# Kernel tuning notes

Hardware: AMD Instinct MI355X
Metric: run time of the kernel (lower is better)

The kernel has to match this reference:

```python
import jax, jax.numpy as jnp
import numpy as np

B, L, E, D, H, P, NL = 4, 2048, 7, 512, 8, 720, 2
DH = D // H
FACTOR = 5
U = min(L, FACTOR * int(np.ceil(np.log(L))))  # top-u queries, = 40
SCALE = 1.0 / np.sqrt(DH)


def setup_inputs() -> dict:
    key = jax.random.key(0)
    ks = jax.random.split(key, 12)
    s = 0.02
    rn = lambda k, shape: jax.random.normal(k, shape, jnp.float32) * s
    return {
        "x": jax.random.normal(ks[0], (B, L, E), jnp.float32),
        "emb_w": rn(ks[1], (E, D)), "emb_b": jnp.zeros((D,), jnp.float32),
        "Wq": rn(ks[2], (NL, D, D)), "bq": jnp.zeros((NL, D), jnp.float32),
        "Wk": rn(ks[3], (NL, D, D)), "bk": jnp.zeros((NL, D), jnp.float32),
        "Wv": rn(ks[4], (NL, D, D)), "bv": jnp.zeros((NL, D), jnp.float32),
        "Wo": rn(ks[5], (NL, D, D)), "bo": jnp.zeros((NL, D), jnp.float32),
        "W1": rn(ks[6], (NL, D, D)), "b1": jnp.zeros((NL, D), jnp.float32),
        "W2": rn(ks[7], (NL, D, D)), "b2": jnp.zeros((NL, D), jnp.float32),
        "ln1_g": jnp.ones((NL, D), jnp.float32), "ln1_b": jnp.zeros((NL, D), jnp.float32),
        "ln2_g": jnp.ones((NL, D), jnp.float32), "ln2_b": jnp.zeros((NL, D), jnp.float32),
        "proj_w": rn(ks[8], (D, E)), "proj_b": jnp.zeros((E,), jnp.float32),
    }


def layer_norm(x, g, b):
    m = jnp.mean(x, axis=-1, keepdims=True)
    v = jnp.mean(jnp.square(x - m), axis=-1, keepdims=True)
    return (x - m) * jax.lax.rsqrt(v + 1e-5) * g + b


def prob_sparse_attn(x, Wq, bq, Wk, bk, Wv, bv, Wo, bo):
    # x: [B, L, D] -> heads [B, H, L, DH]
    q = (x @ Wq + bq).reshape(B, L, H, DH).transpose(0, 2, 1, 3)
    k = (x @ Wk + bk).reshape(B, L, H, DH).transpose(0, 2, 1, 3)
    v = (x @ Wv + bv).reshape(B, L, H, DH).transpose(0, 2, 1, 3)
    scores = jnp.einsum('bhqd,bhkd->bhqk', q, k) * SCALE  # [B,H,L,L]
    # sparsity measure M(q) = max_k - mean_k
    M = jnp.max(scores, axis=-1) - jnp.mean(scores, axis=-1)  # [B,H,L]
    _, idx = jax.lax.top_k(M, U)  # [B,H,U] indices of active queries
    s_top = jnp.take_along_axis(scores, idx[..., None], axis=2)  # [B,H,U,L]
    attn = jax.nn.softmax(s_top, axis=-1)
    upd = jnp.einsum('bhul,bhld->bhud', attn, v)  # [B,H,U,DH]
    # lazy queries get the mean of V; active queries get attention output
    ctx = jnp.broadcast_to(jnp.mean(v, axis=2, keepdims=True), v.shape)
    bidx = jnp.arange(B)[:, None, None]
    hidx = jnp.arange(H)[None, :, None]
    ctx = ctx.at[bidx, hidx, idx].set(upd)  # scatter active queries
    out = ctx.transpose(0, 2, 1, 3).reshape(B, L, D)
    return out @ Wo + bo


def reference(x, emb_w, emb_b, Wq, bq, Wk, bk, Wv, bv, Wo, bo,
              W1, b1, W2, b2, ln1_g, ln1_b, ln2_g, ln2_b, proj_w, proj_b):
    h = x @ emb_w + emb_b  # [B,L,D]
    for i in range(NL):
        a = prob_sparse_attn(h, Wq[i], bq[i], Wk[i], bk[i], Wv[i], bv[i], Wo[i], bo[i])
        h = layer_norm(h + a, ln1_g[i], ln1_b[i])
        f = jax.nn.relu(h @ W1[i] + b1[i]) @ W2[i] + b2[i]
        h = layer_norm(h + f, ln2_g[i], ln2_b[i])
    return h[:, -P:, :] @ proj_w + proj_b  # [B,P,E]
```

## Files before the change

kernel.cpp:

```cpp
#include <hip/hip_runtime.h>
#include <hip/hip_bf16.h>
#include <cstdint>
#include <cstddef>

#define BB 4
#define LL 2048
#define EE 7
#define DD 512
#define HH 8
#define DHH 64
#define PP 720
#define NLAYER 2
#define UU 40
#define SCALE 0.125f
#define ROWS (BB*LL)
#define BIGN ((size_t)ROWS*DD)
#define NIN 21
#define FCH 256
#define NCH (LL/FCH)
#define PSTR 264
#define VSTR 136
#define WOFF 1280
#define WTPB 12
#define WRPB 768

typedef unsigned short u16;
typedef unsigned long long u64;
typedef __bf16 bf16x8 __attribute__((ext_vector_type(8)));
typedef float  f32x4  __attribute__((ext_vector_type(4)));

__device__ __forceinline__ float bf2f(u16 u){
  union { uint32_t i; float f; } c; c.i = ((uint32_t)u) << 16; return c.f;
}
__device__ __forceinline__ u16 f2b(float f){
  __hip_bfloat16 h = __float2bfloat16(f);
  return *(u16*)&h;
}
__device__ __forceinline__ void gld_lds16(const u16* g, u16* l){
  __builtin_amdgcn_global_load_lds(
      (const __attribute__((address_space(1))) uint32_t*)g,
      (__attribute__((address_space(3))) uint32_t*)l, 16, 0, 0);
}
__device__ __forceinline__ int is_bf16(const void* d15){
  return (*(const uint32_t*)d15 == 0x3F800000u) ? 0 : 1;
}

__device__ __forceinline__ void addln_row_vals(const u16* a, const u16* r,
    const float* g, const float* bvec, int row, int lane, u16 ob[8]){
  size_t base = (size_t)row * DD + lane*8;
  ushort4 a0 = *(const ushort4*)(a + base);
  ushort4 a1 = *(const ushort4*)(a + base + 4);
  ushort4 r0 = *(const ushort4*)(r + base);
  ushort4 r1 = *(const ushort4*)(r + base + 4);
  float x[8] = {bf2f(a0.x)+bf2f(r0.x), bf2f(a0.y)+bf2f(r0.y),
                bf2f(a0.z)+bf2f(r0.z), bf2f(a0.w)+bf2f(r0.w),
                bf2f(a1.x)+bf2f(r1.x), bf2f(a1.y)+bf2f(r1.y),
                bf2f(a1.z)+bf2f(r1.z), bf2f(a1.w)+bf2f(r1.w)};
  float s = 0.f;
  #pragma unroll
  for (int i=0;i<8;i++) s += x[i];
  #pragma unroll
  for (int off=1; off<64; off<<=1) s += __shfl_xor(s, off);
  float mean = s * (1.0f/DD);
  float vs = 0.f;
  #pragma unroll
  for (int i=0;i<8;i++){ x[i] -= mean; vs += x[i]*x[i]; }
  #pragma unroll
  for (int off=1; off<64; off<<=1) vs += __shfl_xor(vs, off);
  float rs = rsqrtf(vs * (1.0f/DD) + 1e-5f);
  const float* gp = g + lane*8;
  const float* bp = bvec + lane*8;
  #pragma unroll
  for (int i=0;i<8;i++) ob[i] = f2b(x[i]*rs*gp[i] + bp[i]);
}

__device__ __forceinline__ void tile_map(int flat, int tilesPerB, int winOff,
                                         int* mbRow, int* nbOut){
  int mq = tilesPerB >> 1;
  int xcd = flat & 7, rest = flat >> 3;
  int mbi = xcd + 8*(rest % mq);
  int bat = mbi / tilesPerB;
  *mbRow = bat*LL + winOff + (mbi - bat*tilesPerB)*64;
  *nbOut = (rest / mq) * 128;
}

#define NSMALL 15
struct ConvArgs { const void* src[NSMALL]; int off[NSMALL]; int n[NSMALL]; };
struct WPtrs { const void* p[6]; };

__global__ __launch_bounds__(256) void k_preamble(ConvArgs a, WPtrs wp,
    const void* __restrict__ xraw, const void* __restrict__ d15,
    float* __restrict__ dst, float* __restrict__ zbuf,
    u16* __restrict__ hB, u16* __restrict__ wT){
  int y = blockIdx.y, bx = blockIdx.x, t = threadIdx.x;
  int isbf = is_bf16(d15);
  __shared__ u16 tile[64][65];
  __shared__ float xs[32][EE];
  if (y < NSMALL){
    int i = bx*256 + t;
    if (i >= a.n[y]) return;
    float v;
    if (isbf) v = bf2f(((const u16*)a.src[y])[i]);
    else      v = ((const float*)a.src[y])[i];
    dst[(size_t)a.off[y] + i] = v;
  } else if (y == NSMALL){
    int i = bx*256 + t;
    if (i < NLAYER*4096) zbuf[i] = 0.f;
  } else if (y < 32){
    int flat = (y - 16)*256 + bx;
    if (flat >= 512) return;
    int colgrp = flat & 1;
    int rowbase = (flat >> 1) * 32;
    int dd = colgrp*256 + t;
    if (t < 32*EE){
      int j = t / EE, e = t - j*EE;
      xs[j][e] = isbf ? bf2f(((const u16*)xraw)[(rowbase + j)*EE + e])
                      : ((const float*)xraw)[(rowbase + j)*EE + e];
    }
    float wreg[EE];
    #pragma unroll
    for (int e=0;e<EE;e++)
      wreg[e] = isbf ? bf2f(((const u16*)a.src[1])[e*DD + dd])
                     : ((const float*)a.src[1])[e*DD + dd];
    float bias = isbf ? bf2f(((const u16*)a.src[2])[dd]) : ((const float*)a.src[2])[dd];
    __syncthreads();
    for (int j=0;j<32;j++){
      float acc = bias;
      #pragma unroll
      for (int e=0;e<EE;e++) acc = fmaf(xs[j][e], wreg[e], acc);
      hB[(size_t)(rowbase + j)*DD + dd] = f2b(acc);
    }
  } else {
    int flat = (y - 32)*256 + bx;
    int mz = flat >> 6, tl = flat & 63;
    int lay = mz / 6, mat = mz % 6;
    int n0 = (tl & 7)*64, k0 = (tl >> 3)*64;
    int r = t >> 6, c = t & 63;
    const void* src = wp.p[mat];
    for (int rr = r; rr < 64; rr += 4){
      size_t idx = ((size_t)lay*DD + (k0+rr))*DD + n0 + c;
      u16 v;
      if (isbf) v = ((const u16*)src)[idx];
      else      v = f2b(((const float*)src)[idx]);
      tile[rr][c] = v;
    }
    __syncthreads();
    u16* drow = wT + ((size_t)mz*DD + n0)*DD + k0;
    int c4 = (t & 15)*4;
    for (int rr = (t >> 4); rr < 64; rr += 16){
      ushort4 v = { tile[c4][rr], tile[c4+1][rr], tile[c4+2][rr], tile[c4+3][rr] };
      *(ushort4*)(drow + (size_t)rr*DD + c4) = v;
    }
  }
}

__global__ __launch_bounds__(256) void k_gemm_mfma(const u16* __restrict__ A, const u16* __restrict__ Bt,
    const float* __restrict__ bias, u16* __restrict__ Cb, int relu,
    int tilesPerB, int winOff){
  __shared__ u16 As[64*64];
  __shared__ u16 Bs[128*64];
  int t = threadIdx.x, wave = t >> 6, lane = t & 63;
  int qlane = lane & 15, quad = lane >> 4;
  int flat = blockIdx.x + gridDim.x*blockIdx.y;
  int mb, nb;
  tile_map(flat, tilesPerB, winOff, &mb, &nb);
  int wm = (wave & 1) * 32, wn = (wave >> 1) * 64;
  f32x4 acc[2][4];
  #pragma unroll
  for (int i=0;i<2;i++)
    #pragma unroll
    for (int j=0;j<4;j++) acc[i][j] = (f32x4){0.f,0.f,0.f,0.f};

  int srow = wave*8 + (lane>>3);
  int scol = (((lane&7) ^ ((lane>>3)&7))) * 8;
  const u16* Ag = A + (size_t)(mb + srow)*DD + scol;
  const u16* Bg = Bt + (size_t)(nb + srow)*DD + scol;

  for (int k0 = 0; k0 < DD; k0 += 64){
    __syncthreads();
    #pragma unroll
    for (int i=0;i<2;i++)
      gld_lds16(Ag + (size_t)i*32*DD + k0, As + (i*32 + wave*8)*64);
    #pragma unroll
    for (int i=0;i<4;i++)
      gld_lds16(Bg + (size_t)i*32*DD + k0, Bs + (i*32 + wave*8)*64);
    __syncthreads();
    #pragma unroll
    for (int ch=0; ch<2; ++ch){
      bf16x8 af[2], bfv[4];
      int cgL = ((ch*4 + quad) ^ (qlane & 7)) * 8;
      #pragma unroll
      for (int i=0;i<2;i++) af[i] = *(const bf16x8*)(As + (wm + i*16 + qlane)*64 + cgL);
      #pragma unroll
      for (int j=0;j<4;j++) bfv[j] = *(const bf16x8*)(Bs + (wn + j*16 + qlane)*64 + cgL);
      #pragma unroll
      for (int i=0;i<2;i++)
        #pragma unroll
        for (int j=0;j<4;j++)
          acc[i][j] = __builtin_amdgcn_mfma_f32_16x16x32_bf16(af[i], bfv[j], acc[i][j], 0, 0, 0);
    }
  }
  #pragma unroll
  for (int i=0;i<2;i++){
    int rbase = mb + wm + i*16 + quad*4;
    #pragma unroll
    for (int j=0;j<4;j++){
      int col = nb + wn + j*16 + qlane;
      float bv = bias[col];
      #pragma unroll
      for (int r=0;r<4;r++){
        float cv = acc[i][j][r] + bv;
        if (relu) cv = fmaxf(cv, 0.f);
        Cb[(size_t)(rbase + r)*DD + col] = f2b(cv);
      }
    }
  }
}

__global__ __launch_bounds__(256) void k_gemm_wo(const u64* __restrict__ rowPtr, const u16* __restrict__ Bt,
    const float* __restrict__ bias, u16* __restrict__ Cb,
    int tilesPerB, int winOff){
  __shared__ u16 As[64*64];
  __shared__ u16 Bs[128*64];
  int t = threadIdx.x, wave = t >> 6, lane = t & 63;
  int qlane = lane & 15, quad = lane >> 4;
  int flat = blockIdx.x + gridDim.x*blockIdx.y;
  int mb, nb;
  tile_map(flat, tilesPerB, winOff, &mb, &nb);
  int wm = (wave & 1) * 32, wn = (wave >> 1) * 64;
  f32x4 acc[2][4];
  #pragma unroll
  for (int i=0;i<2;i++)
    #pragma unroll
    for (int j=0;j<4;j++) acc[i][j] = (f32x4){0.f,0.f,0.f,0.f};

  int srow = wave*8 + (lane>>3);
  int scol = (((lane&7) ^ ((lane>>3)&7))) * 8;
  const u16* Bg = Bt + (size_t)(nb + srow)*DD + scol;

  for (int k0 = 0; k0 < DD; k0 += 64){
    int slice = k0 >> 6;
    __syncthreads();
    #pragma unroll
    for (int i=0;i<2;i++){
      int arow = mb + i*32 + srow;
      const u16* src = (const u16*)(uintptr_t)rowPtr[(size_t)arow*8 + slice] + scol;
      gld_lds16(src, As + (i*32 + wave*8)*64);
    }
    #pragma unroll
    for (int i=0;i<4;i++)
      gld_lds16(Bg + (size_t)i*32*DD + k0, Bs + (i*32 + wave*8)*64);
    __syncthreads();
    #pragma unroll
    for (int ch=0; ch<2; ++ch){
      bf16x8 af[2], bfv[4];
      int cgL = ((ch*4 + quad) ^ (qlane & 7)) * 8;
      #pragma unroll
      for (int i=0;i<2;i++) af[i] = *(const bf16x8*)(As + (wm + i*16 + qlane)*64 + cgL);
      #pragma unroll
      for (int j=0;j<4;j++) bfv[j] = *(const bf16x8*)(Bs + (wn + j*16 + qlane)*64 + cgL);
      #pragma unroll
      for (int i=0;i<2;i++)
        #pragma unroll
        for (int j=0;j<4;j++)
          acc[i][j] = __builtin_amdgcn_mfma_f32_16x16x32_bf16(af[i], bfv[j], acc[i][j], 0, 0, 0);
    }
  }
  #pragma unroll
  for (int i=0;i<2;i++){
    int rbase = mb + wm + i*16 + quad*4;
    #pragma unroll
    for (int j=0;j<4;j++){
      int col = nb + wn + j*16 + qlane;
      float bv = bias[col];
      #pragma unroll
      for (int r=0;r<4;r++){
        float cv = acc[i][j][r] + bv;
        Cb[(size_t)(rbase + r)*DD + col] = f2b(cv);
      }
    }
  }
}

__global__ __launch_bounds__(256) void k_gemm_qkv(const u16* __restrict__ A, const u16* __restrict__ Wt,
    const float* __restrict__ bq, const float* __restrict__ bk, const float* __restrict__ bv,
    u16* __restrict__ qB, u16* __restrict__ kB, u16* __restrict__ vB,
    float* __restrict__ ksum, float* __restrict__ vsum){
  __shared__ u16 As[128*64];
  __shared__ u16 Bs[128*64];
  int t = threadIdx.x, wave = t >> 6, lane = t & 63;
  int qlane = lane & 15, quad = lane >> 4;
  int flat = blockIdx.x + gridDim.x*blockIdx.y;
  int xcd = flat & 7, rest = flat >> 3;
  int mb  = (xcd + 8*(rest & 7)) * 128;
  int nbg = (rest >> 3) * 128;
  int sel = nbg >> 9;
  int nb  = nbg & 511;
  const float* bias = (sel==0) ? bq : (sel==1) ? bk : bv;
  u16* out = (sel==0) ? qB : (sel==1) ? kB : vB;
  const u16* Bt = Wt + (size_t)sel*DD*DD;
  int wm = (wave & 1) * 64, wn = (wave >> 1) * 64;
  f32x4 acc[4][4];
  #pragma unroll
  for (int i=0;i<4;i++)
    #pragma unroll
    for (int j=0;j<4;j++) acc[i][j] = (f32x4){0.f,0.f,0.f,0.f};

  int srow = wave*8 + (lane>>3);
  int scol = (((lane&7) ^ ((lane>>3)&7))) * 8;
  const u16* Ag = A + (size_t)(mb + srow)*DD + scol;
  const u16* Bg = Bt + (size_t)(nb + srow)*DD + scol;

  for (int k0 = 0; k0 < DD; k0 += 64){
    __syncthreads();
    #pragma unroll
    for (int i=0;i<4;i++){
      gld_lds16(Ag + (size_t)i*32*DD + k0, As + (i*32 + wave*8)*64);
      gld_lds16(Bg + (size_t)i*32*DD + k0, Bs + (i*32 + wave*8)*64);
    }
    __syncthreads();
    #pragma unroll
    for (int ch=0; ch<2; ++ch){
      bf16x8 af[4], bf[4];
      int cgL = ((ch*4 + quad) ^ (qlane & 7)) * 8;
      #pragma unroll
      for (int i=0;i<4;i++) af[i] = *(const bf16x8*)(As + (wm + i*16 + qlane)*64 + cgL);
      #pragma unroll
      for (int j=0;j<4;j++) bf[j] = *(const bf16x8*)(Bs + (wn + j*16 + qlane)*64 + cgL);
      #pragma unroll
      for (int i=0;i<4;i++)
        #pragma unroll
        for (int j=0;j<4;j++)
          acc[i][j] = __builtin_amdgcn_mfma_f32_16x16x32_bf16(af[i], bf[j], acc[i][j], 0, 0, 0);
    }
  }
  float csum[4] = {0.f,0.f,0.f,0.f};
  #pragma unroll
  for (int j=0;j<4;j++){
    int col = nb + wn + j*16 + qlane;
    float bvv = bias[col];
    #pragma unroll
    for (int i=0;i<4;i++){
      int rbase = mb + wm + i*16 + quad*4;
      #pragma unroll
      for (int r=0;r<4;r++){
        float cv = acc[i][j][r] + bvv;
        out[(size_t)(rbase + r)*DD + col] = f2b(cv);
        csum[j] += cv;
      }
    }
  }
  if (sel > 0){
    float* dst = (sel==1) ? ksum : vsum;
    int bidx = mb >> 11;
    #pragma unroll
    for (int j=0;j<4;j++){
      float v = csum[j];
      v += __shfl_xor(v, 16);
      v += __shfl_xor(v, 32);
      if ((lane>>4) == 0)
        atomicAdd(dst + bidx*512 + nb + wn + j*16 + lane, v);
    }
  }
}

__global__ __launch_bounds__(256) void k_sparsity_mfma(const u16* __restrict__ qB, const u16* __restrict__ kB,
    const float* __restrict__ ksum, float* __restrict__ Mout){
  int flat = blockIdx.x + gridDim.x*blockIdx.y;
  int xcd = flat & 7, rest = flat >> 3;
  int qc = rest & 15;
  int bh = (rest >> 4)*8 + xcd;
  int b = bh >> 3, hh = bh & 7;
  int q0 = qc * 128;
  int t = threadIdx.x, wave = t >> 6, lane = t & 63;
  const u16* qbase = qB + ((size_t)(b*LL + q0))*DD + hh*DHH;
  const u16* kbase = kB + ((size_t)b*LL)*DD + hh*DHH;
  bf16x8 qa[8][2];
  #pragma unroll
  for (int i=0;i<8;i++)
    #pragma unroll
    for (int c=0;c<2;c++)
      qa[i][c] = *(const bf16x8*)(qbase + (size_t)(i*16 + (lane&15))*DD + c*32 + (lane>>4)*8);
  float rmax[8][4];
  #pragma unroll
  for (int i=0;i<8;i++)
    #pragma unroll
    for (int r=0;r<4;r++) rmax[i][r] = -3.0e38f;
  for (int kt = wave*16; kt < LL; kt += 64){
    bf16x8 kb0 = *(const bf16x8*)(kbase + (size_t)(kt + (lane&15))*DD + (lane>>4)*8);
    bf16x8 kb1 = *(const bf16x8*)(kbase + (size_t)(kt + (lane&15))*DD + 32 + (lane>>4)*8);
    #pragma unroll
    for (int i=0;i<8;i++){
      f32x4 a = (f32x4){0.f,0.f,0.f,0.f};
      a = __builtin_amdgcn_mfma_f32_16x16x32_bf16(qa[i][0], kb0, a, 0, 0, 0);
      a = __builtin_amdgcn_mfma_f32_16x16x32_bf16(qa[i][1], kb1, a, 0, 0, 0);
      #pragma unroll
      for (int r=0;r<4;r++) rmax[i][r] = fmaxf(rmax[i][r], a[r]);
    }
  }
  #pragma unroll
  for (int i=0;i<8;i++)
    #pragma unroll
    for (int r=0;r<4;r++){
      float v = rmax[i][r];
      v = fmaxf(v, __shfl_xor(v, 1));
      v = fmaxf(v, __shfl_xor(v, 2));
      v = fmaxf(v, __shfl_xor(v, 4));
      v = fmaxf(v, __shfl_xor(v, 8));
      rmax[i][r] = v;
    }
  __shared__ float smax[4][128];
  if ((lane & 15) == 0){
    #pragma unroll
    for (int i=0;i<8;i++)
      #pragma unroll
      for (int r=0;r<4;r++)
        smax[wave][i*16 + (lane>>4)*4 + r] = rmax[i][r];
  }
  __syncthreads();
  if (t < 128){
    float mx = fmaxf(fmaxf(smax[0][t], smax[1][t]), fmaxf(smax[2][t], smax[3][t]));
    const u16* qrow = qB + (size_t)(b*LL + q0 + t)*DD + hh*DHH;
    float dot = 0.f;
    #pragma unroll
    for (int dv=0; dv<16; ++dv){
      ushort4 qv = *(const ushort4*)(qrow + dv*4);
      const float* kp = ksum + bh*DHH + dv*4;
      dot += bf2f(qv.x)*kp[0] + bf2f(qv.y)*kp[1]
           + bf2f(qv.z)*kp[2] + bf2f(qv.w)*kp[3];
    }
    Mout[bh*LL + q0 + t] = SCALE * (mx - dot * (1.0f/LL));
  }
}

__global__ __launch_bounds__(256) void k_flash(const u16* __restrict__ qB, const u16* __restrict__ kB,
    const u16* __restrict__ vB, const float* __restrict__ Mv, int* __restrict__ sidx,
    float* __restrict__ pO, float* __restrict__ pM, float* __restrict__ pS){
  int bh = blockIdx.y, c = blockIdx.x;
  int b = bh >> 3, hh = bh & 7;
  int t = threadIdx.x, w = t >> 6, lane = t & 63;
  int qlane = lane & 15, quad = lane >> 4;
  int l0 = c * FCH;
  __shared__ u16 Ps[48*PSTR];
  __shared__ union { uint32_t keys[LL]; u16 vst[64*VSTR]; } uu;
  __shared__ float wred[4][48];
  __shared__ float mrow[48];
  __shared__ int hist[256];
  __shared__ int scr[2];
  __shared__ int tieIdx[64];
  __shared__ int counters[2];
  __shared__ int sidxL[UU], sidxS[UU];

  {
    const float* src = Mv + (size_t)bh*LL;
    #pragma unroll
    for (int j = 0; j < 8; ++j){
      int idx = t + j*256;
      uint32_t u = __float_as_uint(src[idx]);
      uu.keys[idx] = (u & 0x80000000u) ? ~u : (u | 0x80000000u);
    }
    uint32_t prefix = 0, pmask = 0;
    int need = UU;
    #pragma unroll
    for (int pass = 0; pass < 4; ++pass){
      int shift = 24 - pass*8;
      __syncthreads();
      hist[t] = 0;
      __syncthreads();
      #pragma unroll
      for (int j = 0; j < 8; ++j){
        uint32_t k = uu.keys[t + j*256];
        if ((k & pmask) == prefix)
          atomicAdd(&hist[(k >> shift) & 0xFF], 1);
      }
      __syncthreads();
      if (t < 64){
        int ln = t;
        int h0 = hist[ln*4+0], h1 = hist[ln*4+1], h2 = hist[ln*4+2], h3 = hist[ln*4+3];
        int s = h0 + h1 + h2 + h3;
        int acc = s;
        #pragma unroll
        for (int off = 1; off < 64; off <<= 1){
          int v = __shfl_down(acc, off);
          if (ln + off < 64) acc += v;
        }
        int c3 = acc - s;
        int c2 = c3 + h3;
        int c1 = c2 + h2;
        int c0 = c1 + h1;
        if      (need > c3 && need <= c3 + h3){ scr[0] = ln*4+3; scr[1] = c3; }
        else if (need > c2 && need <= c2 + h2){ scr[0] = ln*4+2; scr[1] = c2; }
        else if (need > c1 && need <= c1 + h1){ scr[0] = ln*4+1; scr[1] = c1; }
        else if (need > c0 && need <= c0 + h0){ scr[0] = ln*4+0; scr[1] = c0; }
      }
      __syncthreads();
      prefix |= ((uint32_t)scr[0]) << shift;
      need -= scr[1];
      pmask |= 0xFFu << shift;
    }
    if (t < 2) counters[t] = 0;
    __syncthreads();
    uint32_t Tkey = prefix;
    #pragma unroll
    for (int j = 0; j < 8; ++j){
      int idx = t + j*256;
      uint32_t k = uu.keys[idx];
      if (k > Tkey){
        int p = atomicAdd(&counters[0], 1);
        sidxL[p] = idx;
      } else if (k == Tkey){
        int p = atomicAdd(&counters[1], 1);
        if (p < 64) tieIdx[p] = idx;
      }
    }
    __syncthreads();
    if (t == 0){
      int c_gt = counters[0];
      int tc = counters[1];
      int needTies = UU - c_gt;
      if (tc <= 64){
        for (int m = 0; m < needTies; ++m){
          int bestv = 0x7FFFFFFF, bestp = -1;
          for (int q = 0; q < tc; ++q)
            if (tieIdx[q] < bestv){ bestv = tieIdx[q]; bestp = q; }
          sidxL[c_gt + m] = bestv;
          tieIdx[bestp] = 0x7FFFFFFF;
        }
      } else {
        int m = 0;
        for (int j = 0; j < LL && m < needTies; ++j)
          if (uu.keys[j] == Tkey){ sidxL[c_gt + m] = j; m++; }
      }
    }
    __syncthreads();
    int vv = 0, rk = 0;
    if (t < UU){
      vv = sidxL[t];
      #pragma unroll 8
      for (int j = 0; j < UU; ++j) rk += (sidxL[j] < vv) ? 1 : 0;
    }
    __syncthreads();
    if (t < UU) sidxS[rk] = vv;
    __syncthreads();
    if (c == 0 && t < UU) sidx[bh*UU + t] = sidxS[t];
  }

  const u16* kbase = kB + (size_t)b*LL*DD + hh*DHH;
  const u16* vbase = vB + (size_t)b*LL*DD + hh*DHH;
  const u16* qbase = qB + (size_t)b*LL*DD + hh*DHH;

  bf16x8 qa[3][2];
  #pragma unroll
  for (int i=0;i<3;i++){
    int u = i*16 + qlane;
    if (u < UU){
      const u16* qr = qbase + (size_t)sidxS[u]*DD + quad*8;
      qa[i][0] = *(const bf16x8*)qr;
      qa[i][1] = *(const bf16x8*)(qr + 32);
    } else {
      bf16x8 z;
      #pragma unroll
      for (int q8=0;q8<8;q8++) z[q8] = (__bf16)0.0f;
      qa[i][0] = z; qa[i][1] = z;
    }
  }
  f32x4 S[3][4];
  #pragma unroll
  for (int j=0;j<4;j++){
    const u16* kr = kbase + (size_t)(l0 + w*64 + j*16 + qlane)*DD + quad*8;
    bf16x8 k0 = *(const bf16x8*)kr;
    bf16x8 k1 = *(const bf16x8*)(kr + 32);
    #pragma unroll
    for (int i=0;i<3;i++){
      f32x4 a = (f32x4){0.f,0.f,0.f,0.f};
      a = __builtin_amdgcn_mfma_f32_16x16x32_bf16(qa[i][0], k0, a, 0, 0, 0);
      a = __builtin_amdgcn_mfma_f32_16x16x32_bf16(qa[i][1], k1, a, 0, 0, 0);
      S[i][j] = a;
    }
  }
  #pragma unroll
  for (int i=0;i<3;i++){
    #pragma unroll
    for (int r=0;r<4;r++){
      float m = -3.0e38f;
      #pragma unroll
      for (int j=0;j<4;j++){ S[i][j][r] *= SCALE; m = fmaxf(m, S[i][j][r]); }
      m = fmaxf(m, __shfl_xor(m, 1));
      m = fmaxf(m, __shfl_xor(m, 2));
      m = fmaxf(m, __shfl_xor(m, 4));
      m = fmaxf(m, __shfl_xor(m, 8));
      if (qlane == 0) wred[w][i*16 + quad*4 + r] = m;
    }
  }
  __syncthreads();
  if (t < 48) mrow[t] = fmaxf(fmaxf(wred[0][t], wred[1][t]), fmaxf(wred[2][t], wred[3][t]));
  __syncthreads();
  #pragma unroll
  for (int i=0;i<3;i++){
    #pragma unroll
    for (int r=0;r<4;r++){
      int row = i*16 + quad*4 + r;
      float m = mrow[row];
      float ls = 0.f;
      #pragma unroll
      for (int j=0;j<4;j++){
        float e = __expf(S[i][j][r] - m);
        ls += e;
        Ps[row*PSTR + w*64 + j*16 + qlane] = f2b(e);
      }
      ls += __shfl_xor(ls, 1);
      ls += __shfl_xor(ls, 2);
      ls += __shfl_xor(ls, 4);
      ls += __shfl_xor(ls, 8);
      if (qlane == 0) wred[w][row] = ls;
    }
  }
  __syncthreads();
  if (t < 48){
    pM[(bh*NCH + c)*48 + t] = mrow[t];
    pS[(bh*NCH + c)*48 + t] = wred[0][t] + wred[1][t] + wred[2][t] + wred[3][t];
  }
  f32x4 O[3];
  #pragma unroll
  for (int i=0;i<3;i++) O[i] = (f32x4){0.f,0.f,0.f,0.f};
  for (int half = 0; half < 2; ++half){
    __syncthreads();
    for (int idx = t; idx < 128*64; idx += 256){
      int rr = idx >> 6, d = idx & 63;
      uu.vst[d*VSTR + rr] = vbase[(size_t)(l0 + half*128 + rr)*DD + d];
    }
    __syncthreads();
    #pragma unroll
    for (int ks = 0; ks < 4; ++ks){
      int kloc = half*128 + ks*32;
      bf16x8 bfv = *(const bf16x8*)(uu.vst + (w*16 + qlane)*VSTR + ks*32 + quad*8);
      #pragma unroll
      for (int i=0;i<3;i++){
        bf16x8 af = *(const bf16x8*)(Ps + (i*16 + qlane)*PSTR + kloc + quad*8);
        O[i] = __builtin_amdgcn_mfma_f32_16x16x32_bf16(af, bfv, O[i], 0, 0, 0);
      }
    }
  }
  size_t ob = (size_t)(bh*NCH + c)*48*64;
  #pragma unroll
  for (int i=0;i<3;i++)
    #pragma unroll
    for (int r=0;r<4;r++)
      pO[ob + (size_t)(i*16 + quad*4 + r)*64 + w*16 + qlane] = O[i][r];
}

__global__ __launch_bounds__(256) void k_flash_red(const float* __restrict__ pO, const float* __restrict__ pM,
    const float* __restrict__ pS, const int* __restrict__ sidx, const float* __restrict__ vsum,
    u16* __restrict__ attnC, u16* __restrict__ vmeanB, u64* __restrict__ rowPtr){
  int bh = blockIdx.x; int b = bh >> 3, hh = bh & 7;
  int t = threadIdx.x;
  if (t < 64) vmeanB[b*512 + hh*64 + t] = f2b(vsum[b*512 + hh*64 + t] * (1.0f/LL));
  u64 vmPtr = (u64)(uintptr_t)(vmeanB + b*512 + hh*64);
  for (int row = t; row < LL; row += 256)
    rowPtr[((size_t)b*LL + row)*8 + hh] = vmPtr;
  __syncthreads();
  if (t < UU)
    rowPtr[((size_t)b*LL + sidx[bh*UU + t])*8 + hh] =
        (u64)(uintptr_t)(attnC + ((size_t)bh*UU + t)*64);
  for (int idx = t; idx < UU*64; idx += 256){
    int u = idx >> 6, n = idx & 63;
    float m = -3.0e38f;
    #pragma unroll
    for (int c=0;c<NCH;c++) m = fmaxf(m, pM[(bh*NCH + c)*48 + u]);
    float s = 0.f, o = 0.f;
    #pragma unroll
    for (int c=0;c<NCH;c++){
      float wgt = __expf(pM[(bh*NCH + c)*48 + u] - m);
      s += wgt * pS[(bh*NCH + c)*48 + u];
      o += wgt * pO[((size_t)(bh*NCH + c)*48 + u)*64 + n];
    }
    attnC[((size_t)bh*UU + u)*64 + n] = f2b(o / s);
  }
}

__global__ __launch_bounds__(256) void k_addln(const u16* __restrict__ a, const u16* __restrict__ r,
    const float* __restrict__ g, const float* __restrict__ bvec, u16* __restrict__ outB,
    int rowsPerB, int winOff){
  int g0 = blockIdx.x*4 + (threadIdx.x >> 6);
  int lane = threadIdx.x & 63;
  int bat = g0 / rowsPerB;
  int row = bat*LL + winOff + (g0 - bat*rowsPerB);
  u16 ob[8];
  addln_row_vals(a, r, g, bvec, row, lane, ob);
  size_t base = (size_t)row * DD + lane*8;
  *(ushort4*)(outB + base)     = (ushort4){ob[0],ob[1],ob[2],ob[3]};
  *(ushort4*)(outB + base + 4) = (ushort4){ob[4],ob[5],ob[6],ob[7]};
}

__global__ __launch_bounds__(256) void k_proj_ln(const u16* __restrict__ hIn, const u16* __restrict__ res,
    const float* __restrict__ lng, const float* __restrict__ lnbv,
    const float* __restrict__ pw, const float* __restrict__ pb,
    void* __restrict__ out, const void* __restrict__ d15){
  int w = threadIdx.x >> 6, lane = threadIdx.x & 63;
  int rp = blockIdx.x*4 + w;
  int b = rp / PP, pp = rp - b*PP;
  int row = b*LL + (LL-PP) + pp;
  u16 ob[8];
  addln_row_vals(hIn, res, lng, lnbv, row, lane, ob);
  float x[8];
  #pragma unroll
  for (int j=0;j<8;j++) x[j] = bf2f(ob[j]);
  float acc[EE];
  #pragma unroll
  for (int e=0;e<EE;e++) acc[e]=0.f;
  #pragma unroll
  for (int j=0;j<8;j++){
    const float* wrow = pw + (size_t)(lane*8 + j)*EE;
    #pragma unroll
    for (int e=0;e<EE;e++) acc[e] = fmaf(x[j], wrow[e], acc[e]);
  }
  int isbf = is_bf16(d15);
  #pragma unroll
  for (int e=0;e<EE;e++){
    float rr = acc[e];
    #pragma unroll
    for (int off=32; off>0; off>>=1) rr += __shfl_down(rr, off);
    if (lane == 0){
      float val = rr + pb[e];
      if (isbf) ((__hip_bfloat16*)out)[(size_t)rp*EE + e] = __float2bfloat16(val);
      else      ((float*)out)[(size_t)rp*EE + e] = val;
    }
  }
}

extern "C" void kernel_launch(void* const* d_in, const int* in_sizes, int n_in,
                              void* d_out, int out_size, void* d_ws, size_t ws_size,
                              hipStream_t stream){
  float* ws    = (float*)d_ws;
  float* Mv    = ws;
  float* ksumL = Mv + (size_t)BB*HH*LL;
  float* pM    = ksumL + NLAYER*4096;
  float* pS    = pM + 12288;
  float* pO    = pS + 12288;
  int*   sidx  = (int*)(pO + 786432);
  u64*   rowPtr= (u64*)(((uintptr_t)(sidx + 1280) + 15) & ~(uintptr_t)15);
  u16*   attnC = (u16*)(rowPtr + (size_t)ROWS*8);
  u16*   vmeanB= attnC + (size_t)BB*HH*UU*64;
  u16*   hB    = vmeanB + 2048;
  u16*   qB    = hB + BIGN;
  u16*   kB    = qB + BIGN;
  u16*   vB    = kB + BIGN;
  u16*   f1B   = vB + BIGN;
  u16*   tmpB  = f1B + BIGN;
  u16*   wT    = tmpB + BIGN;
  float* conv  = (float*)(((uintptr_t)(wT + (size_t)12*DD*DD) + 15) & ~(uintptr_t)15);

  static const int small_ids[NSMALL] = {0,1,2,4,6,8,10,12,14,15,16,17,18,19,20};
  ConvArgs ca;
  int off_all[NIN];
  int tot = 0;
  for (int i = 0; i < NIN; ++i) off_all[i] = -1;
  for (int s = 0; s < NSMALL; ++s){
    int i = small_ids[s];
    ca.src[s] = d_in[i];
    ca.off[s] = tot;
    ca.n[s]   = in_sizes[i];
    off_all[i] = tot;
    tot += in_sizes[i];
  }
  const float* bq = conv + off_all[4];
  const float* bk = conv + off_all[6];
  const float* bv = conv + off_all[8];
  const float* bo = conv + off_all[10];
  const float* b1 = conv + off_all[12];
  const float* b2 = conv + off_all[14];
  const float* ln1g = conv + off_all[15]; const float* ln1b = conv + off_all[16];
  const float* ln2g = conv + off_all[17]; const float* ln2b = conv + off_all[18];
  const float* pw = conv + off_all[19]; const float* pb = conv + off_all[20];

  WPtrs wp;
  wp.p[0]=d_in[3]; wp.p[1]=d_in[5]; wp.p[2]=d_in[7];
  wp.p[3]=d_in[9]; wp.p[4]=d_in[11]; wp.p[5]=d_in[13];

  k_preamble<<<dim3(256, 35), 256, 0, stream>>>(ca, wp, d_in[0], d_in[15],
                                                conv, ksumL, hB, wT);

  dim3 gg0(4, 128);
  dim3 gg1(4, WTPB*BB);
  dim3 gq(3*DD/128, ROWS/128);

  for (int l = 0; l < NLAYER; ++l){
    const u16* WqkvT = wT + (size_t)(l*6 + 0)*DD*DD;
    const u16* WoT   = wT + (size_t)(l*6 + 3)*DD*DD;
    const u16* W1T   = wT + (size_t)(l*6 + 4)*DD*DD;
    const u16* W2T   = wT + (size_t)(l*6 + 5)*DD*DD;
    float* ksum = ksumL + l*4096;
    float* vsum = ksum + 2048;

    k_gemm_qkv<<<gq, 256, 0, stream>>>(hB, WqkvT, bq + l*DD, bk + l*DD, bv + l*DD,
                                       qB, kB, vB, ksum, vsum);
    k_sparsity_mfma<<<dim3(LL/128, BB*HH), 256, 0, stream>>>(qB, kB, ksum, Mv);
    k_flash<<<dim3(NCH, BB*HH), 256, 0, stream>>>(qB, kB, vB, Mv, sidx, pO, pM, pS);
    k_flash_red<<<BB*HH, 256, 0, stream>>>(pO, pM, pS, sidx, vsum, attnC, vmeanB, rowPtr);
    if (l < NLAYER - 1){
      k_gemm_wo<<<gg0, 256, 0, stream>>>(rowPtr, WoT, bo + l*DD, tmpB, 32, 0);
      k_addln<<<ROWS/4, 256, 0, stream>>>(hB, tmpB, ln1g + l*DD, ln1b + l*DD, hB, LL, 0);
      k_gemm_mfma<<<gg0, 256, 0, stream>>>(hB, W1T, b1 + l*DD, f1B, 1, 32, 0);
      k_gemm_mfma<<<gg0, 256, 0, stream>>>(f1B, W2T, b2 + l*DD, tmpB, 0, 32, 0);
      k_addln<<<ROWS/4, 256, 0, stream>>>(hB, tmpB, ln2g + l*DD, ln2b + l*DD, hB, LL, 0);
    } else {
      k_gemm_wo<<<gg1, 256, 0, stream>>>(rowPtr, WoT, bo + l*DD, tmpB, WTPB, WOFF);
      k_addln<<<(WRPB*BB)/4, 256, 0, stream>>>(hB, tmpB, ln1g + l*DD, ln1b + l*DD, hB,
                                               WRPB, WOFF);
      k_gemm_mfma<<<gg1, 256, 0, stream>>>(hB, W1T, b1 + l*DD, f1B, 1, WTPB, WOFF);
      k_gemm_mfma<<<gg1, 256, 0, stream>>>(f1B, W2T, b2 + l*DD, tmpB, 0, WTPB, WOFF);
      k_proj_ln<<<(BB*PP)/4, 256, 0, stream>>>(hB, tmpB, ln2g + l*DD, ln2b + l*DD,
                                               pw, pb, d_out, d_in[15]);
    }
  }
}
```

Baseline: 348.2 us.

## Fuse Q/K/V tiles per block in QKV GEMM and vectorize V staging

The QKV GEMM used 128x128 tiles, each covering one of Q, K or V. Now each block computes a 128-row by 64-column tile for all three at once, so the A tile is loaded once and reused across the Q, K and V weights. The grid goes from 12x64 to 8x64 blocks, each with more work, and the kernel holds 24 accumulators in place of 16, which may raise register pressure. Separately, the V transpose staging in the flash kernel now reads 8 elements per thread with vector loads instead of scalar loads.

```diff
diff --git a/kernel.cpp b/kernel.cpp
--- a/kernel.cpp
+++ b/kernel.cpp
@@ -287,79 +287,88 @@
     u16* __restrict__ qB, u16* __restrict__ kB, u16* __restrict__ vB,
     float* __restrict__ ksum, float* __restrict__ vsum){
   __shared__ u16 As[128*64];
-  __shared__ u16 Bs[128*64];
+  __shared__ u16 Bs[3][64*64];
   int t = threadIdx.x, wave = t >> 6, lane = t & 63;
   int qlane = lane & 15, quad = lane >> 4;
   int flat = blockIdx.x + gridDim.x*blockIdx.y;
   int xcd = flat & 7, rest = flat >> 3;
   int mb  = (xcd + 8*(rest & 7)) * 128;
-  int nbg = (rest >> 3) * 128;
-  int sel = nbg >> 9;
-  int nb  = nbg & 511;
-  const float* bias = (sel==0) ? bq : (sel==1) ? bk : bv;
-  u16* out = (sel==0) ? qB : (sel==1) ? kB : vB;
-  const u16* Bt = Wt + (size_t)sel*DD*DD;
-  int wm = (wave & 1) * 64, wn = (wave >> 1) * 64;
-  f32x4 acc[4][4];
-  #pragma unroll
-  for (int i=0;i<4;i++)
-    #pragma unroll
-    for (int j=0;j<4;j++) acc[i][j] = (f32x4){0.f,0.f,0.f,0.f};
+  int nb  = (rest >> 3) * 64;
+  int wm  = wave * 32;
+  f32x4 acc[3][2][4];
+  #pragma unroll
+  for (int s=0;s<3;s++)
+    #pragma unroll
+    for (int i=0;i<2;i++)
+      #pragma unroll
+      for (int j=0;j<4;j++) acc[s][i][j] = (f32x4){0.f,0.f,0.f,0.f};
 
   int srow = wave*8 + (lane>>3);
   int scol = (((lane&7) ^ ((lane>>3)&7))) * 8;
   const u16* Ag = A + (size_t)(mb + srow)*DD + scol;
-  const u16* Bg = Bt + (size_t)(nb + srow)*DD + scol;
+  const u16* Bg = Wt + (size_t)(nb + srow)*DD + scol;
 
   for (int k0 = 0; k0 < DD; k0 += 64){
     __syncthreads();
     #pragma unroll
-    for (int i=0;i<4;i++){
+    for (int i=0;i<4;i++)
       gld_lds16(Ag + (size_t)i*32*DD + k0, As + (i*32 + wave*8)*64);
-      gld_lds16(Bg + (size_t)i*32*DD + k0, Bs + (i*32 + wave*8)*64);
-    }
+    #pragma unroll
+    for (int s=0;s<3;s++)
+      #pragma unroll
+      for (int i=0;i<2;i++)
+        gld_lds16(Bg + (size_t)s*DD*DD + (size_t)i*32*DD + k0, Bs[s] + (i*32 + wave*8)*64);
     __syncthreads();
     #pragma unroll
     for (int ch=0; ch<2; ++ch){
-      bf16x8 af[4], bf[4];
       int cgL = ((ch*4 + quad) ^ (qlane & 7)) * 8;
-      #pragma unroll
-      for (int i=0;i<4;i++) af[i] = *(const bf16x8*)(As + (wm + i*16 + qlane)*64 + cgL);
-      #pragma unroll
-      for (int j=0;j<4;j++) bf[j] = *(const bf16x8*)(Bs + (wn + j*16 + qlane)*64 + cgL);
-      #pragma unroll
-      for (int i=0;i<4;i++)
+      bf16x8 af[2];
+      #pragma unroll
+      for (int i=0;i<2;i++) af[i] = *(const bf16x8*)(As + (wm + i*16 + qlane)*64 + cgL);
+      #pragma unroll
+      for (int s=0;s<3;s++){
+        bf16x8 bf[4];
         #pragma unroll
-        for (int j=0;j<4;j++)
-          acc[i][j] = __builtin_amdgcn_mfma_f32_16x16x32_bf16(af[i], bf[j], acc[i][j], 0, 0, 0);
-    }
-  }
-  float csum[4] = {0.f,0.f,0.f,0.f};
-  #pragma unroll
-  for (int j=0;j<4;j++){
-    int col = nb + wn + j*16 + qlane;
-    float bvv = bias[col];
-    #pragma unroll
-    for (int i=0;i<4;i++){
-      int rbase = mb + wm + i*16 + quad*4;
-      #pragma unroll
-      for (int r=0;r<4;r++){
-        float cv = acc[i][j][r] + bvv;
-        out[(size_t)(rbase + r)*DD + col] = f2b(cv);
-        csum[j] += cv;
-      }
-    }
-  }
-  if (sel > 0){
-    float* dst = (sel==1) ? ksum : vsum;
-    int bidx = mb >> 11;
+        for (int j=0;j<4;j++) bf[j] = *(const bf16x8*)(Bs[s] + (j*16 + qlane)*64 + cgL);
+        #pragma unroll
+        for (int i=0;i<2;i++)
+          #pragma unroll
+          for (int j=0;j<4;j++)
+            acc[s][i][j] = __builtin_amdgcn_mfma_f32_16x16x32_bf16(af[i], bf[j], acc[s][i][j], 0, 0, 0);
+      }
+    }
+  }
+  #pragma unroll
+  for (int s=0;s<3;s++){
+    const float* bias = (s==0) ? bq : (s==1) ? bk : bv;
+    u16* out = (s==0) ? qB : (s==1) ? kB : vB;
+    float csum[4] = {0.f,0.f,0.f,0.f};
     #pragma unroll
     for (int j=0;j<4;j++){
-      float v = csum[j];
-      v += __shfl_xor(v, 16);
-      v += __shfl_xor(v, 32);
-      if ((lane>>4) == 0)
-        atomicAdd(dst + bidx*512 + nb + wn + j*16 + lane, v);
+      int col = nb + j*16 + qlane;
+      float bvv = bias[col];
+      #pragma unroll
+      for (int i=0;i<2;i++){
+        int rbase = mb + wm + i*16 + quad*4;
+        #pragma unroll
+        for (int r=0;r<4;r++){
+          float cv = acc[s][i][j][r] + bvv;
+          out[(size_t)(rbase + r)*DD + col] = f2b(cv);
+          csum[j] += cv;
+        }
+      }
+    }
+    if (s > 0){
+      float* dst = (s==1) ? ksum : vsum;
+      int bidx = mb >> 11;
+      #pragma unroll
+      for (int j=0;j<4;j++){
+        float v = csum[j];
+        v += __shfl_xor(v, 16);
+        v += __shfl_xor(v, 32);
+        if ((lane>>4) == 0)
+          atomicAdd(dst + bidx*512 + nb + j*16 + lane, v);
+      }
     }
   }
 }
@@ -625,9 +634,16 @@
   for (int i=0;i<3;i++) O[i] = (f32x4){0.f,0.f,0.f,0.f};
   for (int half = 0; half < 2; ++half){
     __syncthreads();
-    for (int idx = t; idx < 128*64; idx += 256){
-      int rr = idx >> 6, d = idx & 63;
-      uu.vst[d*VSTR + rr] = vbase[(size_t)(l0 + half*128 + rr)*DD + d];
+    for (int idx = t; idx < 128*8; idx += 256){
+      int rr = idx >> 3, d8 = idx & 7;
+      const u16* src = vbase + (size_t)(l0 + half*128 + rr)*DD + d8*8;
+      ushort4 v0 = *(const ushort4*)src;
+      ushort4 v1 = *(const ushort4*)(src + 4);
+      int d = d8*8;
+      uu.vst[(d+0)*VSTR + rr] = v0.x; uu.vst[(d+1)*VSTR + rr] = v0.y;
+      uu.vst[(d+2)*VSTR + rr] = v0.z; uu.vst[(d+3)*VSTR + rr] = v0.w;
+      uu.vst[(d+4)*VSTR + rr] = v1.x; uu.vst[(d+5)*VSTR + rr] = v1.y;
+      uu.vst[(d+6)*VSTR + rr] = v1.z; uu.vst[(d+7)*VSTR + rr] = v1.w;
     }
     __syncthreads();
     #pragma unroll
@@ -782,7 +798,7 @@
 
   dim3 gg0(4, 128);
   dim3 gg1(4, WTPB*BB);
-  dim3 gq(3*DD/128, ROWS/128);
+  dim3 gq(8, 64);
 
   for (int l = 0; l < NLAYER; ++l){
     const u16* WqkvT = wT + (size_t)(l*6 + 0)*DD*DD;
```

New measurement: 345.3 us. Within noise of the previous version (-0.8%).
